# Kernel optimization log

Hardware: AMD Instinct MI355X
Metric: run time of the kernel (lower is better)

The kernel has to match this reference:

```python
import jax, jax.numpy as jnp
import numpy as np

N, M, H, EMB, F = 2000, 32, 64, 32, 32   # nodes, neighbors, hidden, emb_dim, node_feat_dim
T, B, HOR = 12, 4, 12                     # seq_len, batch, horizon
K = 2                                     # tcn kernel
L_SAGE = 2
DILS = (1, 2)                             # dilations for the 2 TCN blocks


def _causal_conv(x, w, b, d):
    # x: (BN, C, T), w: (C_out, C_in, K) -- causal via left padding (K-1)*d
    y = jax.lax.conv_general_dilated(
        x, w, window_strides=(1,), padding=[((K - 1) * d, 0)],
        rhs_dilation=(d,), dimension_numbers=('NCH', 'OIH', 'NCH'))
    return y + b[None, :, None]


def setup_inputs() -> dict:
    key = jax.random.key(0)
    ks = jax.random.split(key, 32)
    s = 0.05
    def g(i, shape):
        return jax.random.normal(ks[i], shape, dtype=jnp.float32) * s
    return dict(
        inputs=jax.random.normal(ks[0], (T, B, N), dtype=jnp.float32),
        node_feas=jax.random.normal(ks[1], (N, F), dtype=jnp.float32),
        node_index=jax.random.randint(ks[2], (N, M), 0, N),
        # NodeEmbeddingMLP (fc3/fc4/fc5)
        w_fc3=g(3, (F, H)), b_fc3=jnp.zeros((H,), jnp.float32),
        w_fc4=g(4, (H, H)), b_fc4=jnp.zeros((H,), jnp.float32),
        w_fc5=g(5, (H, EMB)), b_fc5=jnp.zeros((EMB,), jnp.float32),
        # node_hidden_proj
        w_nhp=g(6, (EMB, H)), b_nhp=jnp.zeros((H,), jnp.float32),
        # attention (no bias)
        w_q=g(7, (EMB, H)), w_k=g(8, (EMB, H)),
        # input_proj
        w_in=g(9, (1, H)), b_in=jnp.zeros((H,), jnp.float32),
        # GraphSAGE layers (stacked)
        sage_w_self=g(10, (L_SAGE, H, H)), sage_b_self=jnp.zeros((L_SAGE, H), jnp.float32),
        sage_w_neigh=g(11, (L_SAGE, H, H)), sage_b_neigh=jnp.zeros((L_SAGE, H), jnp.float32),
        # TCN: 2 temporal blocks, each with conv1/conv2 (OIH layout)
        tcn_w1=g(12, (2, H, H, K)), tcn_b1=jnp.zeros((2, H), jnp.float32),
        tcn_w2=g(13, (2, H, H, K)), tcn_b2=jnp.zeros((2, H), jnp.float32),
        # scalar gate + output head
        w_gate=g(14, (H, 1)), b_gate=jnp.zeros((1,), jnp.float32),
        w_out=g(15, (H, HOR)), b_out=jnp.zeros((HOR,), jnp.float32),
    )


def reference(inputs, node_feas, node_index,
              w_fc3, b_fc3, w_fc4, b_fc4, w_fc5, b_fc5,
              w_nhp, b_nhp, w_q, w_k, w_in, b_in,
              sage_w_self, sage_b_self, sage_w_neigh, sage_b_neigh,
              tcn_w1, tcn_b1, tcn_w2, tcn_b2,
              w_gate, b_gate, w_out, b_out):
    # --- node embedding MLP ---
    e = jax.nn.relu(node_feas @ w_fc3 + b_fc3)
    e = jax.nn.relu(e @ w_fc4 + b_fc4)
    e = e @ w_fc5 + b_fc5                                  # (N, EMB)

    # --- attention over sampled neighbors (learned slim adjacency) ---
    q = e @ w_q                                            # (N, H)
    k = e[node_index] @ w_k                                # (N, M, H)
    scores = jnp.einsum('nh,nmh->nm', q, k) / jnp.sqrt(jnp.float32(H))
    w_adj = jax.nn.softmax(scores, axis=1)                 # (N, M) rows sum to 1

    node_hidden = e @ w_nhp + b_nhp                        # (N, H)

    # --- reshape inputs: (T, B, N) -> (B, T, N, 1) ---
    x = jnp.transpose(inputs, (1, 0, 2)).reshape(B, T, N, 1)
    x_proj = x @ w_in + b_in                               # (B, T, N, H)
    fused = x_proj + node_hidden                           # broadcast (N, H)
    h = fused.reshape(B * T, N, H)

    # --- GraphSAGE encoder: gather neighbors, weighted aggregate ---
    for l in range(L_SAGE):
        nb = h[:, node_index]                              # (B*T, N, M, H) irregular gather
        agg = jnp.einsum('nm,bnmh->bnh', w_adj, nb)        # (B*T, N, H)
        h = jax.nn.relu(h @ sage_w_self[l] + sage_b_self[l]
                        + agg @ sage_w_neigh[l] + sage_b_neigh[l])

    mid_output = h.reshape(B, T, N, H)

    # --- TCN over time per node: (B*N, H, T) ---
    ht = jnp.transpose(mid_output, (0, 2, 3, 1)).reshape(B * N, H, T)
    for l in range(2):
        res = ht
        y = jax.nn.relu(_causal_conv(ht, tcn_w1[l], tcn_b1[l], DILS[l]))
        y = jax.nn.relu(_causal_conv(y, tcn_w2[l], tcn_b2[l], DILS[l]))
        ht = jax.nn.relu(y + res)

    h_t = ht[:, :, -1]                                     # (B*N, H) last step temporal
    h_s = mid_output[:, -1].reshape(B * N, H)              # (B*N, H) last step spatial
    gate = jax.nn.sigmoid(h_t @ w_gate + b_gate)           # (B*N, 1) scalar gate
    fused_out = gate * h_t + (1.0 - gate) * h_s

    out = fused_out @ w_out + b_out                        # (B*N, HOR)
    outputs = out.reshape(B, N, HOR).transpose(2, 0, 1).reshape(HOR, B, N)
    return outputs, mid_output, w_adj
```

## Files before the change

kernel.cpp:

```cpp
#include <hip/hip_runtime.h>
#include <math.h>


__global__ __launch_bounds__(256) void k_embed(
    const float* __restrict__ nf, const float* __restrict__ inputs,
    const float* __restrict__ w3, const float* __restrict__ b3,
    const float* __restrict__ w4, const float* __restrict__ b4,
    const float* __restrict__ w5, const float* __restrict__ b5,
    const float* __restrict__ wq, const float* __restrict__ wk,
    const float* __restrict__ wn, const float* __restrict__ bn,
    const float* __restrict__ b_in,
    const float* __restrict__ tw1, const float* __restrict__ tw2,
    const float* __restrict__ sws, const float* __restrict__ swn,
    float2* __restrict__ W2, float4* __restrict__ wsg,
    float* __restrict__ qo, float* __restrict__ eko, float* __restrict__ nho,
    float* __restrict__ xT)
{
    const int tid = threadIdx.x;
    if (tid < 192) {
        const int id = blockIdx.x * 192 + tid;
        const int t = id / 8000, rem = id % 8000;
        const int b = rem / 2000, n2 = rem % 2000;
        xT[n2 * 48 + b * 12 + t] = inputs[id];
    }
    if (blockIdx.x < 64) {
        const int id = blockIdx.x * 256 + tid;
        const int pr = id & 1, half = (id >> 1) & 1;
        const int ig = (id >> 2) & 15, c = (id >> 6) & 3, o = id >> 8;
        const float* src = (c == 0) ? tw1 : (c == 1) ? tw2
                         : (c == 2) ? tw1 + 8192 : tw2 + 8192;
        const int i = ig * 4 + half * 2 + pr;
        W2[id] = make_float2(src[o * 128 + i * 2], src[o * 128 + i * 2 + 1]);
    } else if (blockIdx.x < 80) {
        const int id = (blockIdx.x - 64) * 256 + tid;
        const int l = id >> 11, rr = id & 2047;
        const int k2 = rr >> 6, h = rr & 63;
        const float* S = sws + l * 4096;
        const float* Nn = swn + l * 4096;
        wsg[id] = make_float4(S[(2 * k2) * 64 + h],     Nn[(2 * k2) * 64 + h],
                              S[(2 * k2 + 1) * 64 + h], Nn[(2 * k2 + 1) * 64 + h]);
    }
    const int lane = tid & 63;
    const int n = blockIdx.x * 4 + (tid >> 6);

    float nfv = 0.f;
    if (lane < 32) nfv = nf[n * 32 + lane];

    float e1 = b3[lane];
#pragma unroll
    for (int f = 0; f < 32; ++f)
        e1 = fmaf(__shfl(nfv, f), w3[f * 64 + lane], e1);
    e1 = fmaxf(e1, 0.f);

    float e2 = b4[lane];
#pragma unroll
    for (int f = 0; f < 64; ++f)
        e2 = fmaf(__shfl(e1, f), w4[f * 64 + lane], e2);
    e2 = fmaxf(e2, 0.f);

    const int c = lane & 31;
    float ev = b5[c];
#pragma unroll
    for (int f = 0; f < 64; ++f)
        ev = fmaf(__shfl(e2, f), w5[f * 32 + c], ev);

    float qv = 0.f, ekv = 0.f, nhv = bn[lane] + b_in[lane];
#pragma unroll
    for (int f = 0; f < 32; ++f) {
        float e = __shfl(ev, f);
        qv  = fmaf(e, wq[f * 64 + lane], qv);
        ekv = fmaf(e, wk[f * 64 + lane], ekv);
        nhv = fmaf(e, wn[f * 64 + lane], nhv);
    }
    qo [n * 64 + lane] = qv;
    eko[n * 64 + lane] = ekv;
    nho[n * 64 + lane] = nhv;
}

__global__ __launch_bounds__(256) void k_front(
    const float* __restrict__ q, const float* __restrict__ ek,
    const float* __restrict__ xT, const float* __restrict__ nh2,
    const int* __restrict__ nidx,
    const float* __restrict__ sws, const float* __restrict__ sbs,
    const float* __restrict__ swn, const float* __restrict__ sbn,
    const float* __restrict__ w_in, const float4* __restrict__ wsg,
    float* __restrict__ wadj, float2* __restrict__ xa,
    float* __restrict__ base1, float* __restrict__ vecs)
{
    const int tid = threadIdx.x;
    const int lane = tid & 63, wave = tid >> 6;
    if (blockIdx.x == 500) {
        if (wave == 0) {
            const float wv = w_in[lane];
            float s1 = 0.f, n1 = 0.f;
#pragma unroll
            for (int k = 0; k < 64; ++k) {
                const float wkk = __shfl(wv, k);
                s1 = fmaf(wkk, sws[k * 64 + lane], s1);
                n1 = fmaf(wkk, swn[k * 64 + lane], n1);
            }
            vecs[lane] = s1; vecs[64 + lane] = n1;
        }
        return;
    }
    __shared__ __align__(16) float2 pair[4][64];
    const int n = blockIdx.x * 4 + wave;

    int j = 0;
    if (lane < 32) j = nidx[n * 32 + lane];
    float w;
    {
        const float4* qr = (const float4*)(q + n * 64);
        const float4* er = (const float4*)(ek + j * 64);
        float s = 0.f;
#pragma unroll
        for (int u = 0; u < 16; ++u) {
            const float4 a = qr[u], b = er[u];
            s = fmaf(a.x, b.x, s); s = fmaf(a.y, b.y, s);
            s = fmaf(a.z, b.z, s); s = fmaf(a.w, b.w, s);
        }
        s *= 0.125f;
        float mx = s;
#pragma unroll
        for (int d = 16; d >= 1; d >>= 1) mx = fmaxf(mx, __shfl_xor(mx, d));
        const float ex = expf(s - mx);
        float sum = ex;
#pragma unroll
        for (int d = 16; d >= 1; d >>= 1) sum += __shfl_xor(sum, d);
        w = ex / sum;
        if (lane < 32) wadj[n * 32 + lane] = w;
    }
    float ax = 0.f, anh = 0.f;
    const bool act = lane < 48;
#pragma unroll 8
    for (int m = 0; m < 32; ++m) {
        const int jm = __shfl(j, m);
        const float wm = __shfl(w, m);
        const float xv = act ? xT[jm * 48 + lane] : 0.f;
        ax  = fmaf(wm, xv, ax);
        anh = fmaf(wm, nh2[jm * 64 + lane], anh);
    }
    if (act) xa[n * 48 + lane] = make_float2(xT[n * 48 + lane], ax);
    pair[wave][lane] = make_float2(nh2[n * 64 + lane], anh);
    __syncthreads();

    float acc = sbs[lane] + sbn[lane];
    const float2* pw = pair[wave];
#pragma unroll
    for (int k2 = 0; k2 < 32; ++k2) {
        const float4 wv = wsg[k2 * 64 + lane];
        const float4 sv = *(const float4*)(pw + k2 * 2);
        acc = fmaf(sv.x, wv.x, acc); acc = fmaf(sv.y, wv.y, acc);
        acc = fmaf(sv.z, wv.z, acc); acc = fmaf(sv.w, wv.w, acc);
    }
    base1[n * 64 + lane] = acc;
}

__global__ __launch_bounds__(512, 4) void k_sage2(
    const float* __restrict__ base1, const float2* __restrict__ xa,
    const float* __restrict__ vecs,
    const int* __restrict__ nidx, const float* __restrict__ wadj,
    const float4* __restrict__ wsg2,
    const float* __restrict__ sbs, const float* __restrict__ sbn,
    float* __restrict__ mid)
{
    __shared__ __align__(16) float2 svp[48][64];
    const int tid = threadIdx.x, lane = tid & 63;
    const int wave = __builtin_amdgcn_readfirstlane(tid >> 6);
    const int n = blockIdx.x;
    const int bt0 = wave * 6;

    const float s1 = vecs[lane], n1 = vecs[64 + lane];
    const float bs = base1[n * 64 + lane];

    float agg[6] = {0.f, 0.f, 0.f, 0.f, 0.f, 0.f};
#pragma unroll 8
    for (int m = 0; m < 32; ++m) {
        const int j = nidx[n * 32 + m];
        const float w = wadj[n * 32 + m];
        const float bj = base1[j * 64 + lane];
        const float4* xr = (const float4*)(xa + j * 48 + bt0);
        const float4 p0 = xr[0], p1 = xr[1], p2 = xr[2];
        float t;
        t = fmaf(p0.x, s1, fmaf(p0.y, n1, bj)); agg[0] = fmaf(w, fmaxf(t, 0.f), agg[0]);
        t = fmaf(p0.z, s1, fmaf(p0.w, n1, bj)); agg[1] = fmaf(w, fmaxf(t, 0.f), agg[1]);
        t = fmaf(p1.x, s1, fmaf(p1.y, n1, bj)); agg[2] = fmaf(w, fmaxf(t, 0.f), agg[2]);
        t = fmaf(p1.z, s1, fmaf(p1.w, n1, bj)); agg[3] = fmaf(w, fmaxf(t, 0.f), agg[3]);
        t = fmaf(p2.x, s1, fmaf(p2.y, n1, bj)); agg[4] = fmaf(w, fmaxf(t, 0.f), agg[4]);
        t = fmaf(p2.z, s1, fmaf(p2.w, n1, bj)); agg[5] = fmaf(w, fmaxf(t, 0.f), agg[5]);
    }
    {
        const float4* xs = (const float4*)(xa + n * 48 + bt0);
        const float4 q0 = xs[0], q1 = xs[1], q2 = xs[2];
        svp[bt0 + 0][lane] = make_float2(fmaxf(fmaf(q0.x, s1, fmaf(q0.y, n1, bs)), 0.f), agg[0]);
        svp[bt0 + 1][lane] = make_float2(fmaxf(fmaf(q0.z, s1, fmaf(q0.w, n1, bs)), 0.f), agg[1]);
        svp[bt0 + 2][lane] = make_float2(fmaxf(fmaf(q1.x, s1, fmaf(q1.y, n1, bs)), 0.f), agg[2]);
        svp[bt0 + 3][lane] = make_float2(fmaxf(fmaf(q1.z, s1, fmaf(q1.w, n1, bs)), 0.f), agg[3]);
        svp[bt0 + 4][lane] = make_float2(fmaxf(fmaf(q2.x, s1, fmaf(q2.y, n1, bs)), 0.f), agg[4]);
        svp[bt0 + 5][lane] = make_float2(fmaxf(fmaf(q2.z, s1, fmaf(q2.w, n1, bs)), 0.f), agg[5]);
    }
    const float b2 = sbs[64 + lane] + sbn[64 + lane];
    float acc[6] = {b2, b2, b2, b2, b2, b2};
    const float4* wp = wsg2 + lane;
    const float2* s0 = svp[bt0];
#pragma unroll
    for (int k2 = 0; k2 < 32; ++k2) {
        const float4 w4 = wp[k2 * 64];
        const float4 v0 = *(const float4*)(s0 + 0 * 64 + k2 * 2);
        const float4 v1 = *(const float4*)(s0 + 1 * 64 + k2 * 2);
        const float4 v2 = *(const float4*)(s0 + 2 * 64 + k2 * 2);
        const float4 v3 = *(const float4*)(s0 + 3 * 64 + k2 * 2);
        const float4 v4 = *(const float4*)(s0 + 4 * 64 + k2 * 2);
        const float4 v5 = *(const float4*)(s0 + 5 * 64 + k2 * 2);
        acc[0] = fmaf(v0.x, w4.x, fmaf(v0.y, w4.y, fmaf(v0.z, w4.z, fmaf(v0.w, w4.w, acc[0]))));
        acc[1] = fmaf(v1.x, w4.x, fmaf(v1.y, w4.y, fmaf(v1.z, w4.z, fmaf(v1.w, w4.w, acc[1]))));
        acc[2] = fmaf(v2.x, w4.x, fmaf(v2.y, w4.y, fmaf(v2.z, w4.z, fmaf(v2.w, w4.w, acc[2]))));
        acc[3] = fmaf(v3.x, w4.x, fmaf(v3.y, w4.y, fmaf(v3.z, w4.z, fmaf(v3.w, w4.w, acc[3]))));
        acc[4] = fmaf(v4.x, w4.x, fmaf(v4.y, w4.y, fmaf(v4.z, w4.z, fmaf(v4.w, w4.w, acc[4]))));
        acc[5] = fmaf(v5.x, w4.x, fmaf(v5.y, w4.y, fmaf(v5.z, w4.z, fmaf(v5.w, w4.w, acc[5]))));
    }
#pragma unroll
    for (int r = 0; r < 6; ++r)
        mid[((bt0 + r) * 2000 + n) * 64 + lane] = fmaxf(acc[r], 0.f);
}

__global__ __launch_bounds__(256, 4) void k_tcn(
    const float* __restrict__ mid, const float2* __restrict__ W2,
    const float* __restrict__ tb1, const float* __restrict__ tb2,
    const float* __restrict__ wgate, const float* __restrict__ bgate,
    const float* __restrict__ wout, const float* __restrict__ bout,
    float* __restrict__ outp)
{
    __shared__ __align__(16) float xls[9][8][68];
    const int tid = threadIdx.x, lane = tid & 63;
    const int wfl = __builtin_amdgcn_readfirstlane(tid >> 6);
    const int hg = (lane >> 3) & 7;
    const int s = lane & 7;
    const int bI = blockIdx.x / 250;
    const int n0 = (blockIdx.x - bI * 250) * 8;
    const long base = ((long)(bI * 12) * 2000 + n0) * 64;
    const int obase = wfl * 16 + hg * 2;
    const float4* __restrict__ w0p = (const float4*)W2 + (obase + 0) * 128;
    const float4* __restrict__ w1p = (const float4*)W2 + (obase + 1) * 128;

    for (int e = tid; e < 896; e += 256) {
        const int u = e >> 7, rem = e & 127;
        const int ss = rem >> 4, qq = rem & 15;
        const float4 v = *(const float4*)(mid + base + (5 + u) * 128000L + ss * 64 + qq * 4);
        *(float4*)&xls[u][ss][qq * 4] = v;
    }
    __syncthreads();

    float y[2][6];
    {
        const float2 bv = *(const float2*)(tb1 + obase);
#pragma unroll
        for (int j = 0; j < 6; ++j) { y[0][j] = bv.x; y[1][j] = bv.y; }
    }
#pragma unroll 2
    for (int ig = 0; ig < 16; ++ig) {
        float4 xv[7];
#pragma unroll
        for (int u = 0; u < 7; ++u)
            xv[u] = *(const float4*)&xls[u][s][ig * 4];
#pragma unroll
        for (int oo = 0; oo < 2; ++oo) {
            const float4* wp = oo ? w1p : w0p;
            const float4 wA = wp[ig * 2 + 0];
            const float4 wB = wp[ig * 2 + 1];
#pragma unroll
            for (int j = 0; j < 6; ++j) {
                float acc = y[oo][j];
                acc = fmaf(wA.x, xv[j].x, acc); acc = fmaf(wA.y, xv[j+1].x, acc);
                acc = fmaf(wA.z, xv[j].y, acc); acc = fmaf(wA.w, xv[j+1].y, acc);
                acc = fmaf(wB.x, xv[j].z, acc); acc = fmaf(wB.y, xv[j+1].z, acc);
                acc = fmaf(wB.z, xv[j].w, acc); acc = fmaf(wB.w, xv[j+1].w, acc);
                y[oo][j] = acc;
            }
        }
    }
    __syncthreads();
    {
        const int S1OUT[6] = {0, 1, 7, 3, 8, 5};
#pragma unroll
        for (int j = 0; j < 6; ++j) {
            float2 o2;
            o2.x = fmaxf(y[0][j], 0.f); o2.y = fmaxf(y[1][j], 0.f);
            *(float2*)&xls[S1OUT[j]][s][obase] = o2;
        }
    }
    __syncthreads();

    float a[2][3];
    {
        const float2 bv = *(const float2*)(tb2 + obase);
#pragma unroll
        for (int v = 0; v < 3; ++v) { a[0][v] = bv.x; a[1][v] = bv.y; }
    }
#pragma unroll 2
    for (int ig = 0; ig < 16; ++ig) {
        const float4 y0 = *(const float4*)&xls[0][s][ig * 4];
        const float4 y1v = *(const float4*)&xls[1][s][ig * 4];
        const float4 y2 = *(const float4*)&xls[7][s][ig * 4];
        const float4 y3v = *(const float4*)&xls[3][s][ig * 4];
        const float4 y4 = *(const float4*)&xls[8][s][ig * 4];
        const float4 y5 = *(const float4*)&xls[5][s][ig * 4];
#pragma unroll
        for (int oo = 0; oo < 2; ++oo) {
            const float4* wp = oo ? w1p : w0p;
            const float4 wA = wp[32 + ig * 2 + 0];
            const float4 wB = wp[32 + ig * 2 + 1];
            float t0 = a[oo][0], t1 = a[oo][1], t2 = a[oo][2];
            t0 = fmaf(wA.x, y0.x, t0);  t0 = fmaf(wA.y, y1v.x, t0);
            t0 = fmaf(wA.z, y0.y, t0);  t0 = fmaf(wA.w, y1v.y, t0);
            t0 = fmaf(wB.x, y0.z, t0);  t0 = fmaf(wB.y, y1v.z, t0);
            t0 = fmaf(wB.z, y0.w, t0);  t0 = fmaf(wB.w, y1v.w, t0);
            t1 = fmaf(wA.x, y2.x, t1);  t1 = fmaf(wA.y, y3v.x, t1);
            t1 = fmaf(wA.z, y2.y, t1);  t1 = fmaf(wA.w, y3v.y, t1);
            t1 = fmaf(wB.x, y2.z, t1);  t1 = fmaf(wB.y, y3v.z, t1);
            t1 = fmaf(wB.z, y2.w, t1);  t1 = fmaf(wB.w, y3v.w, t1);
            t2 = fmaf(wA.x, y4.x, t2);  t2 = fmaf(wA.y, y5.x, t2);
            t2 = fmaf(wA.z, y4.y, t2);  t2 = fmaf(wA.w, y5.y, t2);
            t2 = fmaf(wB.x, y4.z, t2);  t2 = fmaf(wB.y, y5.z, t2);
            t2 = fmaf(wB.z, y4.w, t2);  t2 = fmaf(wB.w, y5.w, t2);
            a[oo][0] = t0; a[oo][1] = t1; a[oo][2] = t2;
        }
    }
    __syncthreads();
    {
        const int RIN[3] = {2, 4, 6}, ROUT[3] = {0, 1, 7};
#pragma unroll
        for (int v = 0; v < 3; ++v) {
            const float2 xr = *(const float2*)&xls[RIN[v]][s][obase];
            float2 o2;
            o2.x = fmaxf(fmaxf(a[0][v], 0.f) + xr.x, 0.f);
            o2.y = fmaxf(fmaxf(a[1][v], 0.f) + xr.y, 0.f);
            *(float2*)&xls[ROUT[v]][s][obase] = o2;
        }
    }
    __syncthreads();

    float d[2][2];
    {
        const float2 bv = *(const float2*)(tb1 + 64 + obase);
        d[0][0] = bv.x; d[0][1] = bv.x; d[1][0] = bv.y; d[1][1] = bv.y;
    }
#pragma unroll 2
    for (int ig = 0; ig < 16; ++ig) {
        const float4 x0 = *(const float4*)&xls[0][s][ig * 4];
        const float4 x1 = *(const float4*)&xls[1][s][ig * 4];
        const float4 x2 = *(const float4*)&xls[7][s][ig * 4];
#pragma unroll
        for (int oo = 0; oo < 2; ++oo) {
            const float4* wp = oo ? w1p : w0p;
            const float4 wA = wp[64 + ig * 2 + 0];
            const float4 wB = wp[64 + ig * 2 + 1];
            float t0 = d[oo][0], t1 = d[oo][1];
            t0 = fmaf(wA.x, x0.x, t0);  t0 = fmaf(wA.y, x1.x, t0);
            t0 = fmaf(wA.z, x0.y, t0);  t0 = fmaf(wA.w, x1.y, t0);
            t0 = fmaf(wB.x, x0.z, t0);  t0 = fmaf(wB.y, x1.z, t0);
            t0 = fmaf(wB.z, x0.w, t0);  t0 = fmaf(wB.w, x1.w, t0);
            t1 = fmaf(wA.x, x1.x, t1);  t1 = fmaf(wA.y, x2.x, t1);
            t1 = fmaf(wA.z, x1.y, t1);  t1 = fmaf(wA.w, x2.y, t1);
            t1 = fmaf(wB.x, x1.z, t1);  t1 = fmaf(wB.y, x2.z, t1);
            t1 = fmaf(wB.z, x1.w, t1);  t1 = fmaf(wB.w, x2.w, t1);
            d[oo][0] = t0; d[oo][1] = t1;
        }
    }
    {
        float2 o2;
        o2.x = fmaxf(d[0][0], 0.f); o2.y = fmaxf(d[1][0], 0.f);
        *(float2*)&xls[3][s][obase] = o2;
        o2.x = fmaxf(d[0][1], 0.f); o2.y = fmaxf(d[1][1], 0.f);
        *(float2*)&xls[8][s][obase] = o2;
    }
    __syncthreads();

    float f[2];
    {
        const float2 bv = *(const float2*)(tb2 + 64 + obase);
        f[0] = bv.x; f[1] = bv.y;
    }
#pragma unroll 2
    for (int ig = 0; ig < 16; ++ig) {
        const float4 g0 = *(const float4*)&xls[3][s][ig * 4];
        const float4 g1 = *(const float4*)&xls[8][s][ig * 4];
#pragma unroll
        for (int oo = 0; oo < 2; ++oo) {
            const float4* wp = oo ? w1p : w0p;
            const float4 wA = wp[96 + ig * 2 + 0];
            const float4 wB = wp[96 + ig * 2 + 1];
            float t0 = f[oo];
            t0 = fmaf(wA.x, g0.x, t0);  t0 = fmaf(wA.y, g1.x, t0);
            t0 = fmaf(wA.z, g0.y, t0);  t0 = fmaf(wA.w, g1.y, t0);
            t0 = fmaf(wB.x, g0.z, t0);  t0 = fmaf(wB.y, g1.z, t0);
            t0 = fmaf(wB.z, g0.w, t0);  t0 = fmaf(wB.w, g1.w, t0);
            f[oo] = t0;
        }
    }
    float ht[2];
    {
        const float2 xr = *(const float2*)&xls[7][s][obase];
        ht[0] = fmaxf(fmaxf(f[0], 0.f) + xr.x, 0.f);
        ht[1] = fmaxf(fmaxf(f[1], 0.f) + xr.y, 0.f);
    }

    float* pbuf = &xls[2][0][0];
    {
        const float2 wg2 = *(const float2*)(wgate + obase);
        float p = ht[0] * wg2.x + ht[1] * wg2.y;
        p += __shfl_xor(p, 8); p += __shfl_xor(p, 16); p += __shfl_xor(p, 32);
        if (hg == 0) pbuf[wfl * 8 + s] = p;
    }
    __syncthreads();
    float ptot = 0.f;
#pragma unroll
    for (int w4i = 0; w4i < 4; ++w4i) ptot += pbuf[w4i * 8 + s];
    const float g = 1.f / (1.f + expf(-(ptot + bgate[0])));
    float fo[2];
    {
        const float2 hs = *(const float2*)&xls[6][s][obase];
        fo[0] = g * ht[0] + (1.f - g) * hs.x;
        fo[1] = g * ht[1] + (1.f - g) * hs.y;
    }
    float po[12];
#pragma unroll
    for (int h2 = 0; h2 < 12; ++h2) po[h2] = 0.f;
#pragma unroll
    for (int oo = 0; oo < 2; ++oo) {
        const float* wr = wout + (obase + oo) * 12;
        const float4 w0 = *(const float4*)(wr);
        const float4 w1 = *(const float4*)(wr + 4);
        const float4 w2 = *(const float4*)(wr + 8);
        po[0] = fmaf(fo[oo], w0.x, po[0]);  po[1] = fmaf(fo[oo], w0.y, po[1]);
        po[2] = fmaf(fo[oo], w0.z, po[2]);  po[3] = fmaf(fo[oo], w0.w, po[3]);
        po[4] = fmaf(fo[oo], w1.x, po[4]);  po[5] = fmaf(fo[oo], w1.y, po[5]);
        po[6] = fmaf(fo[oo], w1.z, po[6]);  po[7] = fmaf(fo[oo], w1.w, po[7]);
        po[8] = fmaf(fo[oo], w2.x, po[8]);  po[9] = fmaf(fo[oo], w2.y, po[9]);
        po[10] = fmaf(fo[oo], w2.z, po[10]); po[11] = fmaf(fo[oo], w2.w, po[11]);
    }
#pragma unroll
    for (int h2 = 0; h2 < 12; ++h2) {
        po[h2] += __shfl_xor(po[h2], 8);
        po[h2] += __shfl_xor(po[h2], 16);
        po[h2] += __shfl_xor(po[h2], 32);
    }
    float* pobuf = &xls[4][0][0];
    if (hg == 0) {
#pragma unroll
        for (int h2 = 0; h2 < 12; ++h2)
            pobuf[(wfl * 12 + h2) * 8 + s] = po[h2];
    }
    __syncthreads();
    if (tid < 96) {
        const int h2 = tid >> 3, sq = tid & 7;
        float r = bout[h2];
#pragma unroll
        for (int w4i = 0; w4i < 4; ++w4i)
            r += pobuf[(w4i * 12 + h2) * 8 + sq];
        outp[h2 * 8000 + bI * 2000 + n0 + sq] = r;
    }
}

extern "C" void kernel_launch(void* const* d_in, const int* in_sizes, int n_in,
                              void* d_out, int out_size, void* d_ws, size_t ws_size,
                              hipStream_t stream) {
    const float* inputs     = (const float*)d_in[0];
    const float* node_feas  = (const float*)d_in[1];
    const int*   node_index = (const int*)  d_in[2];
    const float* w_fc3 = (const float*)d_in[3];
    const float* b_fc3 = (const float*)d_in[4];
    const float* w_fc4 = (const float*)d_in[5];
    const float* b_fc4 = (const float*)d_in[6];
    const float* w_fc5 = (const float*)d_in[7];
    const float* b_fc5 = (const float*)d_in[8];
    const float* w_nhp = (const float*)d_in[9];
    const float* b_nhp = (const float*)d_in[10];
    const float* w_q   = (const float*)d_in[11];
    const float* w_k   = (const float*)d_in[12];
    const float* w_in  = (const float*)d_in[13];
    const float* b_in  = (const float*)d_in[14];
    const float* sws   = (const float*)d_in[15];
    const float* sbs   = (const float*)d_in[16];
    const float* swn   = (const float*)d_in[17];
    const float* sbn   = (const float*)d_in[18];
    const float* tw1   = (const float*)d_in[19];
    const float* tb1   = (const float*)d_in[20];
    const float* tw2   = (const float*)d_in[21];
    const float* tb2   = (const float*)d_in[22];
    const float* wgate = (const float*)d_in[23];
    const float* bgate = (const float*)d_in[24];
    const float* wout  = (const float*)d_in[25];
    const float* bout  = (const float*)d_in[26];

    float* out  = (float*)d_out;
    float* mid  = out + 96000;
    float* wadj = mid + 6144000;

    float*  q     = (float*)d_ws;
    float*  ek    = q     + 128000;
    float*  nh2   = ek    + 128000;
    float*  base1 = nh2   + 128000;
    float*  xT    = base1 + 128000;
    float2* xa    = (float2*)(xT + 96000);
    float*  vecs  = xT + 96000 + 192000;
    float2* W2    = (float2*)(vecs + 128);
    float4* wsg   = (float4*)(vecs + 128 + 32768);

    k_embed<<<500, 256, 0, stream>>>(node_feas, inputs, w_fc3, b_fc3, w_fc4, b_fc4,
                                     w_fc5, b_fc5, w_q, w_k, w_nhp, b_nhp, b_in,
                                     tw1, tw2, sws, swn, W2, wsg,
                                     q, ek, nh2, xT);
    k_front<<<501, 256, 0, stream>>>(q, ek, xT, nh2, node_index,
                                     sws, sbs, swn, sbn, w_in, wsg,
                                     wadj, xa, base1, vecs);
    k_sage2<<<2000, 512, 0, stream>>>(base1, xa, vecs, node_index, wadj,
                                      wsg + 2048, sbs, sbn, mid);
    k_tcn<<<1000, 256, 0, stream>>>(mid, W2, tb1, tb2,
                                    wgate, bgate, wout, bout, out);
}
```

Measured before the change: 110.7 us.

## Make TCN kernel wave-private: each wavefront owns two nodes, drop block barriers

The TCN kernel is remapped so that each 64-lane wavefront processes 2 nodes across all 64 output channels, rather than 8 nodes per block with channels split across waves. Each wave gets its own LDS slice, which removes every __syncthreads and the cross-wave LDS reductions for the gate and output head. Those reductions become full-wave shuffle trees instead. In exchange, weight reuse per loaded activation drops (each lane covers only 2 nodes), the number of shuffle steps grows, the global loads become scalar per lane rather than float4, and LDS reads may see more bank conflicts.

```diff
diff --git a/kernel.cpp b/kernel.cpp
--- a/kernel.cpp
+++ b/kernel.cpp
@@ -231,25 +231,24 @@
     const float* __restrict__ wout, const float* __restrict__ bout,
     float* __restrict__ outp)
 {
-    __shared__ __align__(16) float xls[9][8][68];
+    __shared__ __align__(16) float xls[4][9][2][68];
     const int tid = threadIdx.x, lane = tid & 63;
     const int wfl = __builtin_amdgcn_readfirstlane(tid >> 6);
-    const int hg = (lane >> 3) & 7;
-    const int s = lane & 7;
+    const int s = lane & 1;
+    const int hg = lane >> 1;
+    const int obase = hg * 2;
     const int bI = blockIdx.x / 250;
-    const int n0 = (blockIdx.x - bI * 250) * 8;
+    const int n0 = (blockIdx.x - bI * 250) * 8 + wfl * 2;
     const long base = ((long)(bI * 12) * 2000 + n0) * 64;
-    const int obase = wfl * 16 + hg * 2;
     const float4* __restrict__ w0p = (const float4*)W2 + (obase + 0) * 128;
     const float4* __restrict__ w1p = (const float4*)W2 + (obase + 1) * 128;
-
-    for (int e = tid; e < 896; e += 256) {
-        const int u = e >> 7, rem = e & 127;
-        const int ss = rem >> 4, qq = rem & 15;
-        const float4 v = *(const float4*)(mid + base + (5 + u) * 128000L + ss * 64 + qq * 4);
-        *(float4*)&xls[u][ss][qq * 4] = v;
-    }
-    __syncthreads();
+    float (*xw)[2][68] = xls[wfl];
+
+#pragma unroll
+    for (int u = 0; u < 7; ++u) {
+        xw[u][0][lane] = mid[base + (5 + u) * 128000L + lane];
+        xw[u][1][lane] = mid[base + (5 + u) * 128000L + 64 + lane];
+    }
 
     float y[2][6];
     {
@@ -262,7 +261,7 @@
         float4 xv[7];
 #pragma unroll
         for (int u = 0; u < 7; ++u)
-            xv[u] = *(const float4*)&xls[u][s][ig * 4];
+            xv[u] = *(const float4*)&xw[u][s][ig * 4];
 #pragma unroll
         for (int oo = 0; oo < 2; ++oo) {
             const float4* wp = oo ? w1p : w0p;
@@ -279,17 +278,15 @@
             }
         }
     }
-    __syncthreads();
     {
         const int S1OUT[6] = {0, 1, 7, 3, 8, 5};
 #pragma unroll
         for (int j = 0; j < 6; ++j) {
             float2 o2;
             o2.x = fmaxf(y[0][j], 0.f); o2.y = fmaxf(y[1][j], 0.f);
-            *(float2*)&xls[S1OUT[j]][s][obase] = o2;
-        }
-    }
-    __syncthreads();
+            *(float2*)&xw[S1OUT[j]][s][obase] = o2;
+        }
+    }
 
     float a[2][3];
     {
@@ -299,12 +296,12 @@
     }
 #pragma unroll 2
     for (int ig = 0; ig < 16; ++ig) {
-        const float4 y0 = *(const float4*)&xls[0][s][ig * 4];
-        const float4 y1v = *(const float4*)&xls[1][s][ig * 4];
-        const float4 y2 = *(const float4*)&xls[7][s][ig * 4];
-        const float4 y3v = *(const float4*)&xls[3][s][ig * 4];
-        const float4 y4 = *(const float4*)&xls[8][s][ig * 4];
-        const float4 y5 = *(const float4*)&xls[5][s][ig * 4];
+        const float4 y0 = *(const float4*)&xw[0][s][ig * 4];
+        const float4 y1v = *(const float4*)&xw[1][s][ig * 4];
+        const float4 y2 = *(const float4*)&xw[7][s][ig * 4];
+        const float4 y3v = *(const float4*)&xw[3][s][ig * 4];
+        const float4 y4 = *(const float4*)&xw[8][s][ig * 4];
+        const float4 y5 = *(const float4*)&xw[5][s][ig * 4];
 #pragma unroll
         for (int oo = 0; oo < 2; ++oo) {
             const float4* wp = oo ? w1p : w0p;
@@ -326,19 +323,17 @@
             a[oo][0] = t0; a[oo][1] = t1; a[oo][2] = t2;
         }
     }
-    __syncthreads();
     {
         const int RIN[3] = {2, 4, 6}, ROUT[3] = {0, 1, 7};
 #pragma unroll
         for (int v = 0; v < 3; ++v) {
-            const float2 xr = *(const float2*)&xls[RIN[v]][s][obase];
+            const float2 xr = *(const float2*)&xw[RIN[v]][s][obase];
             float2 o2;
             o2.x = fmaxf(fmaxf(a[0][v], 0.f) + xr.x, 0.f);
             o2.y = fmaxf(fmaxf(a[1][v], 0.f) + xr.y, 0.f);
-            *(float2*)&xls[ROUT[v]][s][obase] = o2;
-        }
-    }
-    __syncthreads();
+            *(float2*)&xw[ROUT[v]][s][obase] = o2;
+        }
+    }
 
     float d[2][2];
     {
@@ -347,9 +342,9 @@
     }
 #pragma unroll 2
     for (int ig = 0; ig < 16; ++ig) {
-        const float4 x0 = *(const float4*)&xls[0][s][ig * 4];
-        const float4 x1 = *(const float4*)&xls[1][s][ig * 4];
-        const float4 x2 = *(const float4*)&xls[7][s][ig * 4];
+        const float4 x0 = *(const float4*)&xw[0][s][ig * 4];
+        const float4 x1 = *(const float4*)&xw[1][s][ig * 4];
+        const float4 x2 = *(const float4*)&xw[7][s][ig * 4];
 #pragma unroll
         for (int oo = 0; oo < 2; ++oo) {
             const float4* wp = oo ? w1p : w0p;
@@ -370,11 +365,10 @@
     {
         float2 o2;
         o2.x = fmaxf(d[0][0], 0.f); o2.y = fmaxf(d[1][0], 0.f);
-        *(float2*)&xls[3][s][obase] = o2;
+        *(float2*)&xw[3][s][obase] = o2;
         o2.x = fmaxf(d[0][1], 0.f); o2.y = fmaxf(d[1][1], 0.f);
-        *(float2*)&xls[8][s][obase] = o2;
-    }
-    __syncthreads();
+        *(float2*)&xw[8][s][obase] = o2;
+    }
 
     float f[2];
     {
@@ -383,8 +377,8 @@
     }
 #pragma unroll 2
     for (int ig = 0; ig < 16; ++ig) {
-        const float4 g0 = *(const float4*)&xls[3][s][ig * 4];
-        const float4 g1 = *(const float4*)&xls[8][s][ig * 4];
+        const float4 g0 = *(const float4*)&xw[3][s][ig * 4];
+        const float4 g1 = *(const float4*)&xw[8][s][ig * 4];
 #pragma unroll
         for (int oo = 0; oo < 2; ++oo) {
             const float4* wp = oo ? w1p : w0p;
@@ -398,67 +392,39 @@
             f[oo] = t0;
         }
     }
-    float ht[2];
-    {
-        const float2 xr = *(const float2*)&xls[7][s][obase];
-        ht[0] = fmaxf(fmaxf(f[0], 0.f) + xr.x, 0.f);
-        ht[1] = fmaxf(fmaxf(f[1], 0.f) + xr.y, 0.f);
-    }
-
-    float* pbuf = &xls[2][0][0];
-    {
-        const float2 wg2 = *(const float2*)(wgate + obase);
-        float p = ht[0] * wg2.x + ht[1] * wg2.y;
-        p += __shfl_xor(p, 8); p += __shfl_xor(p, 16); p += __shfl_xor(p, 32);
-        if (hg == 0) pbuf[wfl * 8 + s] = p;
-    }
-    __syncthreads();
-    float ptot = 0.f;
-#pragma unroll
-    for (int w4i = 0; w4i < 4; ++w4i) ptot += pbuf[w4i * 8 + s];
-    const float g = 1.f / (1.f + expf(-(ptot + bgate[0])));
-    float fo[2];
-    {
-        const float2 hs = *(const float2*)&xls[6][s][obase];
-        fo[0] = g * ht[0] + (1.f - g) * hs.x;
-        fo[1] = g * ht[1] + (1.f - g) * hs.y;
-    }
+    float ht0, ht1;
+    {
+        const float2 xr = *(const float2*)&xw[7][s][obase];
+        ht0 = fmaxf(fmaxf(f[0], 0.f) + xr.x, 0.f);
+        ht1 = fmaxf(fmaxf(f[1], 0.f) + xr.y, 0.f);
+    }
+
+    const float2 wg2 = *(const float2*)(wgate + obase);
+    float p = ht0 * wg2.x + ht1 * wg2.y;
+#pragma unroll
+    for (int dd = 2; dd < 64; dd <<= 1) p += __shfl_xor(p, dd);
+    const float g = 1.f / (1.f + expf(-(p + bgate[0])));
+    const float2 hs = *(const float2*)&xw[6][s][obase];
+    const float fo0 = g * ht0 + (1.f - g) * hs.x;
+    const float fo1 = g * ht1 + (1.f - g) * hs.y;
+
     float po[12];
-#pragma unroll
-    for (int h2 = 0; h2 < 12; ++h2) po[h2] = 0.f;
-#pragma unroll
-    for (int oo = 0; oo < 2; ++oo) {
-        const float* wr = wout + (obase + oo) * 12;
-        const float4 w0 = *(const float4*)(wr);
-        const float4 w1 = *(const float4*)(wr + 4);
-        const float4 w2 = *(const float4*)(wr + 8);
-        po[0] = fmaf(fo[oo], w0.x, po[0]);  po[1] = fmaf(fo[oo], w0.y, po[1]);
-        po[2] = fmaf(fo[oo], w0.z, po[2]);  po[3] = fmaf(fo[oo], w0.w, po[3]);
-        po[4] = fmaf(fo[oo], w1.x, po[4]);  po[5] = fmaf(fo[oo], w1.y, po[5]);
-        po[6] = fmaf(fo[oo], w1.z, po[6]);  po[7] = fmaf(fo[oo], w1.w, po[7]);
-        po[8] = fmaf(fo[oo], w2.x, po[8]);  po[9] = fmaf(fo[oo], w2.y, po[9]);
-        po[10] = fmaf(fo[oo], w2.z, po[10]); po[11] = fmaf(fo[oo], w2.w, po[11]);
+    {
+        const float* wr0 = wout + (obase + 0) * 12;
+        const float* wr1 = wout + (obase + 1) * 12;
+#pragma unroll
+        for (int h2 = 0; h2 < 12; ++h2)
+            po[h2] = fo0 * wr0[h2] + fo1 * wr1[h2];
     }
 #pragma unroll
     for (int h2 = 0; h2 < 12; ++h2) {
-        po[h2] += __shfl_xor(po[h2], 8);
-        po[h2] += __shfl_xor(po[h2], 16);
-        po[h2] += __shfl_xor(po[h2], 32);
-    }
-    float* pobuf = &xls[4][0][0];
+#pragma unroll
+        for (int dd = 2; dd < 64; dd <<= 1) po[h2] += __shfl_xor(po[h2], dd);
+    }
     if (hg == 0) {
 #pragma unroll
         for (int h2 = 0; h2 < 12; ++h2)
-            pobuf[(wfl * 12 + h2) * 8 + s] = po[h2];
-    }
-    __syncthreads();
-    if (tid < 96) {
-        const int h2 = tid >> 3, sq = tid & 7;
-        float r = bout[h2];
-#pragma unroll
-        for (int w4i = 0; w4i < 4; ++w4i)
-            r += pobuf[(w4i * 12 + h2) * 8 + sq];
-        outp[h2 * 8000 + bI * 2000 + n0 + sq] = r;
+            outp[h2 * 8000 + bI * 2000 + n0 + s] = po[h2] + bout[h2];
     }
 }
 
```

Result: slower. 130.2 us (+17.6%).
